# Kernel optimization log

Hardware: AMD Instinct MI355X
Metric: run time of the kernel (lower is better)

## Reference

```python
import jax, jax.numpy as jnp
import numpy as np

C = 512
HEADS = 8
B, H, W = 2, 64, 64


def setup_inputs() -> dict:
    key = jax.random.key(0)
    k1, k2, k3, k4, k5 = jax.random.split(key, 5)
    s = 1.0 / np.sqrt(C)
    return {
        "hidden_states": jax.random.normal(k1, (B, C, H, W), dtype=jnp.float32),
        "qkv_w": jax.random.normal(k2, (3 * C, C), dtype=jnp.float32) * s,
        "qkv_b": jax.random.normal(k3, (3 * C,), dtype=jnp.float32) * 0.02,
        "proj_w": jax.random.normal(k4, (C, C), dtype=jnp.float32) * s,
        "proj_b": jax.random.normal(k5, (C,), dtype=jnp.float32) * 0.02,
    }


def reference(hidden_states, qkv_w, qkv_b, proj_w, proj_b):
    b, c, h, w = hidden_states.shape
    n = h * w  # sequence length
    heads = HEADS
    dim_head = c // heads
    scale = dim_head ** -0.5

    x = hidden_states.reshape(b, c, n)  # [b, c, n]
    # 1x1 conv1d == matmul over channel dim
    qkv = jnp.einsum("oc,bcn->bon", qkv_w, x) + qkv_b[None, :, None]  # [b, 3c, n]
    q, k, v = jnp.split(qkv, 3, axis=1)
    # [b, heads, dim_head, n] -> [b, heads, n, dim_head]
    def split_heads(t):
        return t.reshape(b, heads, dim_head, n).transpose(0, 1, 3, 2)
    q, k, v = split_heads(q), split_heads(k), split_heads(v)

    attn = jnp.einsum("bhqd,bhkd->bhqk", q, k) * scale  # [b, heads, n, n]
    attn = jax.nn.softmax(attn, axis=-1)
    out = jnp.einsum("bhqk,bhkd->bhqd", attn, v)  # [b, heads, n, dim_head]
    out = out.transpose(0, 1, 3, 2).reshape(b, c, n)  # [b, c, n]
    out = jnp.einsum("oc,bcn->bon", proj_w, out) + proj_b[None, :, None]
    return out  # [b, c, h*w] (matches torch module, no reshape back)
```

## Files before the change

kernel.cpp:

```cpp
#include <hip/hip_runtime.h>


typedef __attribute__((ext_vector_type(8))) short s16x8;
typedef __attribute__((ext_vector_type(4))) float f32x4;
typedef __attribute__((ext_vector_type(4))) unsigned short u16x4;

__device__ __forceinline__ unsigned short f2bf(float f) {
  unsigned u = __builtin_bit_cast(unsigned, f);
  u += 0x7fffu + ((u >> 16) & 1u);
  return (unsigned short)(u >> 16);
}

__device__ __forceinline__ unsigned cvt_pk_bf16(float lo, float hi) {
  unsigned r;
  asm("v_cvt_pk_bf16_f32 %0, %1, %2" : "=v"(r) : "v"(lo), "v"(hi));
  return r;
}

__global__ __launch_bounds__(256) void prep_weights(
    const float* __restrict__ qkv_w, const float* __restrict__ proj_w,
    short* __restrict__ wq, short* __restrict__ wp) {
  int t = blockIdx.x * 256 + threadIdx.x;
  const int NQ = 1536 * 512 / 4;
  if (t < NQ) {
    float4 v = ((const float4*)qkv_w)[t];
    u16x4 o; o[0] = f2bf(v.x); o[1] = f2bf(v.y); o[2] = f2bf(v.z); o[3] = f2bf(v.w);
    ((u16x4*)wq)[t] = o;
  } else {
    int t2 = t - NQ;
    float4 v = ((const float4*)proj_w)[t2];
    u16x4 o; o[0] = f2bf(v.x); o[1] = f2bf(v.y); o[2] = f2bf(v.z); o[3] = f2bf(v.w);
    ((u16x4*)wp)[t2] = o;
  }
}

__global__ __launch_bounds__(256) void prep_transpose(
    const float* __restrict__ x, short* __restrict__ xt) {
  __shared__ short TL[64 * 72];
  const int b = blockIdx.z, c0 = blockIdx.y * 64, n0 = blockIdx.x * 64;
  const int t = threadIdx.x;
  const int cr = t >> 4, n4 = (t & 15) * 4;
#pragma unroll
  for (int i = 0; i < 4; i++) {
    int c = cr + i * 16;
    float4 v = *(const float4*)(x + ((size_t)(b * 512 + c0 + c)) * 4096 + n0 + n4);
    TL[(n4 + 0) * 72 + c] = (short)f2bf(v.x);
    TL[(n4 + 1) * 72 + c] = (short)f2bf(v.y);
    TL[(n4 + 2) * 72 + c] = (short)f2bf(v.z);
    TL[(n4 + 3) * 72 + c] = (short)f2bf(v.w);
  }
  __syncthreads();
  const int n = t >> 2;
#pragma unroll
  for (int s2 = 0; s2 < 2; s2++) {
    int s = (t & 3) * 2 + s2;
    s16x8 v = *(const s16x8*)&TL[n * 72 + s * 8];
    *(s16x8*)(xt + ((size_t)(b * 4096 + n0 + n)) * 512 + c0 + s * 8) = v;
  }
}

__global__ __launch_bounds__(256) void qkv_gemm(
    const short* __restrict__ wq, const short* __restrict__ xt,
    const float* __restrict__ qkv_b,
    short* __restrict__ qkbuf,
    short* __restrict__ vbuf) {
  __shared__ short Al[128 * 40];
  __shared__ short Bl[128 * 40];
  const int b = blockIdx.z;
  const int m0 = blockIdx.y * 128, n0 = blockIdx.x * 128;
  const bool swapped = (blockIdx.y < 8);
  const int t = threadIdx.x, lane = t & 63, wid = t >> 6;
  const int wr = wid >> 1, wc = wid & 1;
  const int srow = t >> 1, scol = (t & 1) * 16;
  const short* gA = wq + (size_t)(m0 + srow) * 512 + scol;
  const short* gB = xt + ((size_t)(b * 4096 + n0 + srow)) * 512 + scol;
  short* lA = &Al[srow * 40 + scol];
  short* lB = &Bl[srow * 40 + scol];
  const short* As = swapped ? Bl : Al;
  const short* Bs = swapped ? Al : Bl;
  f32x4 acc[4][4] = {};
  for (int ks = 0; ks < 16; ks++) {
    *(s16x8*)lA       = *(const s16x8*)(gA + ks * 32);
    *(s16x8*)(lA + 8) = *(const s16x8*)(gA + ks * 32 + 8);
    *(s16x8*)lB       = *(const s16x8*)(gB + ks * 32);
    *(s16x8*)(lB + 8) = *(const s16x8*)(gB + ks * 32 + 8);
    __syncthreads();
    s16x8 af[4], bf[4];
#pragma unroll
    for (int i = 0; i < 4; i++) {
      af[i] = *(const s16x8*)&As[(wr * 64 + i * 16 + (lane & 15)) * 40 + ((lane >> 4) << 3)];
      bf[i] = *(const s16x8*)&Bs[(wc * 64 + i * 16 + (lane & 15)) * 40 + ((lane >> 4) << 3)];
    }
#pragma unroll
    for (int i = 0; i < 4; i++)
#pragma unroll
      for (int j = 0; j < 4; j++)
        acc[i][j] = __builtin_amdgcn_mfma_f32_16x16x32_bf16(af[i], bf[j], acc[i][j], 0, 0, 0);
    __syncthreads();
  }
  if (!swapped) {
#pragma unroll
    for (int i = 0; i < 4; i++)
#pragma unroll
      for (int r = 0; r < 4; r++) {
        int orow = m0 + wr * 64 + i * 16 + ((lane >> 4) << 2) + r;
        float bias = qkv_b[orow];
#pragma unroll
        for (int j = 0; j < 4; j++) {
          int ncol = n0 + wc * 64 + j * 16 + (lane & 15);
          vbuf[((size_t)(b * 512 + orow - 1024)) * 4096 + ncol] = (short)f2bf(acc[i][j][r] + bias);
        }
      }
  } else {
    const float qs = (m0 < 512) ? 0.18033688f : 1.0f;
#pragma unroll
    for (int j = 0; j < 4; j++) {
      int ocol = m0 + wc * 64 + j * 16 + (lane & 15);
      float bias = qkv_b[ocol];
#pragma unroll
      for (int i = 0; i < 4; i++)
#pragma unroll
        for (int r = 0; r < 4; r++) {
          int nrow = n0 + wr * 64 + i * 16 + ((lane >> 4) << 2) + r;
          qkbuf[((size_t)(b * 4096 + nrow)) * 1024 + ocol] = (short)f2bf((acc[i][j][r] + bias) * qs);
        }
    }
  }
}

__global__ __launch_bounds__(512) void flash_attn(
    const short* __restrict__ qkbuf, const short* __restrict__ vbuf,
    short* __restrict__ aout) {
  __shared__ short Kl[64 * 72];
  __shared__ short Vl[64 * 72];
  __shared__ short Pl[8 * 16 * 72];
  const int t = threadIdx.x, lane = t & 63, wid = t >> 6;
  const int g = lane >> 4, c = lane & 15;
  const int bh = blockIdx.y, b = bh >> 3, h = bh & 7;
  const int qrow = blockIdx.x * 128 + wid * 16 + c;

  s16x8 qf[2];
#pragma unroll
  for (int kd = 0; kd < 2; kd++)
    qf[kd] = *(const s16x8*)(qkbuf + ((size_t)(b * 4096 + qrow)) * 1024
                             + h * 64 + kd * 32 + g * 8);

  f32x4 oacc[4] = {};
  float m = -__builtin_inff();
  float l = 0.f;

  const int srow = t >> 3, sseg = (t & 7) * 8;
  const short* gK = qkbuf + ((size_t)(b * 4096 + srow)) * 1024 + 512 + h * 64 + sseg;
  const short* gV = vbuf + ((size_t)(b * 512 + h * 64 + srow)) * 4096 + sseg;
  short* lK = &Kl[srow * 72 + sseg];
  short* lV = &Vl[srow * 72 + sseg];
  short* myP = &Pl[wid * 16 * 72];

  s16x8 rK = *(const s16x8*)gK;
  s16x8 rV = *(const s16x8*)gV;

  for (int kt = 0; kt < 64; kt++) {
    *(s16x8*)lK = rK;
    *(s16x8*)lV = rV;
    __syncthreads();
    if (kt < 63) {
      rK = *(const s16x8*)(gK + (size_t)(kt + 1) * 64 * 1024);
      rV = *(const s16x8*)(gV + (kt + 1) * 64);
    }
    s16x8 kf[4][2];
#pragma unroll
    for (int ni = 0; ni < 4; ni++)
#pragma unroll
      for (int kd = 0; kd < 2; kd++)
        kf[ni][kd] = *(const s16x8*)&Kl[(ni * 16 + c) * 72 + kd * 32 + g * 8];
    f32x4 st[4] = {};
#pragma unroll
    for (int ni = 0; ni < 4; ni++) {
      st[ni] = __builtin_amdgcn_mfma_f32_16x16x32_bf16(kf[ni][0], qf[0], st[ni], 0, 0, 0);
      st[ni] = __builtin_amdgcn_mfma_f32_16x16x32_bf16(kf[ni][1], qf[1], st[ni], 0, 0, 0);
    }
    float t01 = fmaxf(fmaxf(st[0][0], st[0][1]), fmaxf(st[0][2], st[0][3]));
    float t23 = fmaxf(fmaxf(st[1][0], st[1][1]), fmaxf(st[1][2], st[1][3]));
    float t45 = fmaxf(fmaxf(st[2][0], st[2][1]), fmaxf(st[2][2], st[2][3]));
    float t67 = fmaxf(fmaxf(st[3][0], st[3][1]), fmaxf(st[3][2], st[3][3]));
    float tm = fmaxf(fmaxf(t01, t23), fmaxf(t45, t67));
    tm = fmaxf(tm, __shfl_xor(tm, 16));
    tm = fmaxf(tm, __shfl_xor(tm, 32));
    if (!__all(tm <= m + 8.f)) {
      float mn = fmaxf(m, tm);
      float alpha = exp2f(m - mn);
      m = mn;
      l *= alpha;
#pragma unroll
      for (int di = 0; di < 4; di++)
#pragma unroll
        for (int r = 0; r < 4; r++) oacc[di][r] *= alpha;
    }
    float ps = 0.f;
#pragma unroll
    for (int ni = 0; ni < 4; ni++) {
      float p0 = exp2f(st[ni][0] - m);
      float p1 = exp2f(st[ni][1] - m);
      float p2 = exp2f(st[ni][2] - m);
      float p3 = exp2f(st[ni][3] - m);
      ps += (p0 + p1) + (p2 + p3);
      uint2 w;
      w.x = cvt_pk_bf16(p0, p1);
      w.y = cvt_pk_bf16(p2, p3);
      *(uint2*)&myP[c * 72 + ni * 16 + g * 4] = w;
    }
    l += ps;
#pragma unroll
    for (int ks = 0; ks < 2; ks++) {
      s16x8 pa = *(const s16x8*)&myP[c * 72 + ks * 32 + g * 8];
      s16x8 vbf[4];
#pragma unroll
      for (int di = 0; di < 4; di++)
        vbf[di] = *(const s16x8*)&Vl[(di * 16 + c) * 72 + ks * 32 + g * 8];
#pragma unroll
      for (int di = 0; di < 4; di++)
        oacc[di] = __builtin_amdgcn_mfma_f32_16x16x32_bf16(vbf[di], pa, oacc[di], 0, 0, 0);
    }
    __syncthreads();
  }
  float lf = l;
  lf += __shfl_xor(lf, 16);
  lf += __shfl_xor(lf, 32);
  float inv = 1.f / lf;
#pragma unroll
  for (int di = 0; di < 4; di++)
#pragma unroll
    for (int r = 0; r < 4; r++) {
      int d = di * 16 + g * 4 + r;
      aout[((size_t)(b * 4096 + qrow)) * 512 + h * 64 + d] = (short)f2bf(oacc[di][r] * inv);
    }
}

__global__ __launch_bounds__(256) void proj_gemm(
    const short* __restrict__ wp, const short* __restrict__ aout,
    const float* __restrict__ proj_b, float* __restrict__ out) {
  __shared__ short Al[128 * 40];
  __shared__ short Bl[128 * 40];
  const int b = blockIdx.z;
  const int m0 = blockIdx.y * 128, n0 = blockIdx.x * 128;
  const int t = threadIdx.x, lane = t & 63, wid = t >> 6;
  const int wr = wid >> 1, wc = wid & 1;
  const int srow = t >> 1, scol = (t & 1) * 16;
  const short* gA = wp + (size_t)(m0 + srow) * 512 + scol;
  const short* gB = aout + ((size_t)(b * 4096 + n0 + srow)) * 512 + scol;
  short* lA = &Al[srow * 40 + scol];
  short* lB = &Bl[srow * 40 + scol];
  f32x4 acc[4][4] = {};
  for (int ks = 0; ks < 16; ks++) {
    *(s16x8*)lA       = *(const s16x8*)(gA + ks * 32);
    *(s16x8*)(lA + 8) = *(const s16x8*)(gA + ks * 32 + 8);
    *(s16x8*)lB       = *(const s16x8*)(gB + ks * 32);
    *(s16x8*)(lB + 8) = *(const s16x8*)(gB + ks * 32 + 8);
    __syncthreads();
    s16x8 af[4], bf[4];
#pragma unroll
    for (int i = 0; i < 4; i++) {
      af[i] = *(const s16x8*)&Al[(wr * 64 + i * 16 + (lane & 15)) * 40 + ((lane >> 4) << 3)];
      bf[i] = *(const s16x8*)&Bl[(wc * 64 + i * 16 + (lane & 15)) * 40 + ((lane >> 4) << 3)];
    }
#pragma unroll
    for (int i = 0; i < 4; i++)
#pragma unroll
      for (int j = 0; j < 4; j++)
        acc[i][j] = __builtin_amdgcn_mfma_f32_16x16x32_bf16(af[i], bf[j], acc[i][j], 0, 0, 0);
    __syncthreads();
  }
#pragma unroll
  for (int i = 0; i < 4; i++)
#pragma unroll
    for (int r = 0; r < 4; r++) {
      int orow = m0 + wr * 64 + i * 16 + ((lane >> 4) << 2) + r;
      float bias = proj_b[orow];
#pragma unroll
      for (int j = 0; j < 4; j++) {
        int ncol = n0 + wc * 64 + j * 16 + (lane & 15);
        out[((size_t)(b * 512 + orow)) * 4096 + ncol] = acc[i][j][r] + bias;
      }
    }
}

extern "C" void kernel_launch(void* const* d_in, const int* in_sizes, int n_in,
                              void* d_out, int out_size, void* d_ws, size_t ws_size,
                              hipStream_t stream) {
  const float* x      = (const float*)d_in[0];
  const float* qkv_w  = (const float*)d_in[1];
  const float* qkv_b  = (const float*)d_in[2];
  const float* proj_w = (const float*)d_in[3];
  const float* proj_b = (const float*)d_in[4];
  float* out = (float*)d_out;
  char* ws = (char*)d_ws;
  short* wq = (short*)(ws);
  short* wp = (short*)(ws + 1572864);
  short* xt = (short*)(ws + 2097152);
  short* qk = (short*)(ws + 10485760);
  short* vb = (short*)(ws + 27262976);
  short* ao = (short*)(ws + 35651584);

  prep_weights  <<<1024, 256, 0, stream>>>(qkv_w, proj_w, wq, wp);
  prep_transpose<<<dim3(64, 8, 2), 256, 0, stream>>>(x, xt);
  qkv_gemm      <<<dim3(32, 12, 2), 256, 0, stream>>>(wq, xt, qkv_b, qk, vb);
  flash_attn    <<<dim3(32, 16), 512, 0, stream>>>(qk, vb, ao);
  proj_gemm     <<<dim3(32, 4, 2), 256, 0, stream>>>(wp, ao, proj_b, out);
}
```

Before: 253.8 us.

## Restructure flash attention: direct K/V register loads, 32 query rows per wave, no LDS staging

The flash attention kernel now uses 256-thread blocks in which each wave handles 32 query rows (two 16-row MFMA tiles). K and V tiles are loaded straight from global memory into registers instead of being staged through shared memory behind __syncthreads, which removes the block-wide barriers. Each K/V fragment is reused across both query tiles. The per-wave P buffer uses an XOR swizzle in place of padding, blocks are remapped so heads are interleaved across workgroups, and output stores are packed into 8-byte writes. The cost is that each wave issues its own global loads for K/V (relying on L2 for sharing) and register pressure rises.

```diff
diff --git a/kernel.cpp b/kernel.cpp
--- a/kernel.cpp
+++ b/kernel.cpp
@@ -128,112 +128,117 @@
   }
 }
 
-__global__ __launch_bounds__(512) void flash_attn(
+__global__ __launch_bounds__(256) void flash_attn(
     const short* __restrict__ qkbuf, const short* __restrict__ vbuf,
     short* __restrict__ aout) {
-  __shared__ short Kl[64 * 72];
-  __shared__ short Vl[64 * 72];
-  __shared__ short Pl[8 * 16 * 72];
+  __shared__ short Pl[4 * 32 * 64];
   const int t = threadIdx.x, lane = t & 63, wid = t >> 6;
   const int g = lane >> 4, c = lane & 15;
-  const int bh = blockIdx.y, b = bh >> 3, h = bh & 7;
-  const int qrow = blockIdx.x * 128 + wid * 16 + c;
-
-  s16x8 qf[2];
-#pragma unroll
-  for (int kd = 0; kd < 2; kd++)
-    qf[kd] = *(const s16x8*)(qkbuf + ((size_t)(b * 4096 + qrow)) * 1024
-                             + h * 64 + kd * 32 + g * 8);
-
-  f32x4 oacc[4] = {};
-  float m = -__builtin_inff();
-  float l = 0.f;
-
-  const int srow = t >> 3, sseg = (t & 7) * 8;
-  const short* gK = qkbuf + ((size_t)(b * 4096 + srow)) * 1024 + 512 + h * 64 + sseg;
-  const short* gV = vbuf + ((size_t)(b * 512 + h * 64 + srow)) * 4096 + sseg;
-  short* lK = &Kl[srow * 72 + sseg];
-  short* lV = &Vl[srow * 72 + sseg];
-  short* myP = &Pl[wid * 16 * 72];
-
-  s16x8 rK = *(const s16x8*)gK;
-  s16x8 rV = *(const s16x8*)gV;
+  const int j = blockIdx.x;
+  const int lid = ((j & 7) << 6) + (j >> 3);
+  const int qb = (lid & 31) * 128 + wid * 32;
+  const int bh = lid >> 5, b = bh >> 3, h = bh & 7;
+
+  s16x8 qf[2][2];
+#pragma unroll
+  for (int mi = 0; mi < 2; mi++)
+#pragma unroll
+    for (int kd = 0; kd < 2; kd++)
+      qf[mi][kd] = *(const s16x8*)(qkbuf + ((size_t)(b * 4096 + qb + mi * 16 + c)) * 1024
+                                   + h * 64 + kd * 32 + g * 8);
+
+  f32x4 oacc[2][4] = {};
+  float m[2] = {-__builtin_inff(), -__builtin_inff()};
+  float l[2] = {0.f, 0.f};
+
+  const short* kbase = qkbuf + ((size_t)(b * 4096 + c)) * 1024 + 512 + h * 64 + g * 8;
+  const short* vbase = vbuf + ((size_t)(b * 512 + h * 64 + c)) * 4096 + g * 8;
+  short* myP = &Pl[wid * 32 * 64];
+  const int sw = (c & 7) << 3;
 
   for (int kt = 0; kt < 64; kt++) {
-    *(s16x8*)lK = rK;
-    *(s16x8*)lV = rV;
-    __syncthreads();
-    if (kt < 63) {
-      rK = *(const s16x8*)(gK + (size_t)(kt + 1) * 64 * 1024);
-      rV = *(const s16x8*)(gV + (kt + 1) * 64);
-    }
-    s16x8 kf[4][2];
+    const int kp0 = kt * 64;
+    s16x8 kf[4][2], vf[2][4];
 #pragma unroll
     for (int ni = 0; ni < 4; ni++)
 #pragma unroll
       for (int kd = 0; kd < 2; kd++)
-        kf[ni][kd] = *(const s16x8*)&Kl[(ni * 16 + c) * 72 + kd * 32 + g * 8];
-    f32x4 st[4] = {};
-#pragma unroll
-    for (int ni = 0; ni < 4; ni++) {
-      st[ni] = __builtin_amdgcn_mfma_f32_16x16x32_bf16(kf[ni][0], qf[0], st[ni], 0, 0, 0);
-      st[ni] = __builtin_amdgcn_mfma_f32_16x16x32_bf16(kf[ni][1], qf[1], st[ni], 0, 0, 0);
-    }
-    float t01 = fmaxf(fmaxf(st[0][0], st[0][1]), fmaxf(st[0][2], st[0][3]));
-    float t23 = fmaxf(fmaxf(st[1][0], st[1][1]), fmaxf(st[1][2], st[1][3]));
-    float t45 = fmaxf(fmaxf(st[2][0], st[2][1]), fmaxf(st[2][2], st[2][3]));
-    float t67 = fmaxf(fmaxf(st[3][0], st[3][1]), fmaxf(st[3][2], st[3][3]));
-    float tm = fmaxf(fmaxf(t01, t23), fmaxf(t45, t67));
-    tm = fmaxf(tm, __shfl_xor(tm, 16));
-    tm = fmaxf(tm, __shfl_xor(tm, 32));
-    if (!__all(tm <= m + 8.f)) {
-      float mn = fmaxf(m, tm);
-      float alpha = exp2f(m - mn);
-      m = mn;
-      l *= alpha;
+        kf[ni][kd] = *(const s16x8*)(kbase + (size_t)(kp0 + ni * 16) * 1024 + kd * 32);
+#pragma unroll
+    for (int ks = 0; ks < 2; ks++)
 #pragma unroll
       for (int di = 0; di < 4; di++)
-#pragma unroll
-        for (int r = 0; r < 4; r++) oacc[di][r] *= alpha;
-    }
-    float ps = 0.f;
-#pragma unroll
-    for (int ni = 0; ni < 4; ni++) {
-      float p0 = exp2f(st[ni][0] - m);
-      float p1 = exp2f(st[ni][1] - m);
-      float p2 = exp2f(st[ni][2] - m);
-      float p3 = exp2f(st[ni][3] - m);
-      ps += (p0 + p1) + (p2 + p3);
+        vf[ks][di] = *(const s16x8*)(vbase + (size_t)(di * 16) * 4096 + kp0 + ks * 32);
+#pragma unroll
+    for (int mi = 0; mi < 2; mi++) {
+      f32x4 st[4] = {};
+#pragma unroll
+      for (int ni = 0; ni < 4; ni++) {
+        st[ni] = __builtin_amdgcn_mfma_f32_16x16x32_bf16(kf[ni][0], qf[mi][0], st[ni], 0, 0, 0);
+        st[ni] = __builtin_amdgcn_mfma_f32_16x16x32_bf16(kf[ni][1], qf[mi][1], st[ni], 0, 0, 0);
+      }
+      float t01 = fmaxf(fmaxf(st[0][0], st[0][1]), fmaxf(st[0][2], st[0][3]));
+      float t23 = fmaxf(fmaxf(st[1][0], st[1][1]), fmaxf(st[1][2], st[1][3]));
+      float t45 = fmaxf(fmaxf(st[2][0], st[2][1]), fmaxf(st[2][2], st[2][3]));
+      float t67 = fmaxf(fmaxf(st[3][0], st[3][1]), fmaxf(st[3][2], st[3][3]));
+      float tm = fmaxf(fmaxf(t01, t23), fmaxf(t45, t67));
+      tm = fmaxf(tm, __shfl_xor(tm, 16));
+      tm = fmaxf(tm, __shfl_xor(tm, 32));
+      if (!__all(tm <= m[mi] + 8.f)) {
+        float mn = fmaxf(m[mi], tm);
+        float alpha = exp2f(m[mi] - mn);
+        m[mi] = mn;
+        l[mi] *= alpha;
+#pragma unroll
+        for (int di = 0; di < 4; di++)
+#pragma unroll
+          for (int r = 0; r < 4; r++) oacc[mi][di][r] *= alpha;
+      }
+      float ps = 0.f;
+      const int prow = (mi * 16 + c) * 64;
+#pragma unroll
+      for (int ni = 0; ni < 4; ni++) {
+        float p0 = exp2f(st[ni][0] - m[mi]);
+        float p1 = exp2f(st[ni][1] - m[mi]);
+        float p2 = exp2f(st[ni][2] - m[mi]);
+        float p3 = exp2f(st[ni][3] - m[mi]);
+        ps += (p0 + p1) + (p2 + p3);
+        uint2 w;
+        w.x = cvt_pk_bf16(p0, p1);
+        w.y = cvt_pk_bf16(p2, p3);
+        *(uint2*)&myP[prow + ((ni * 16 + g * 4) ^ sw)] = w;
+      }
+      l[mi] += ps;
+    }
+#pragma unroll
+    for (int ks = 0; ks < 2; ks++) {
+      s16x8 pa[2];
+#pragma unroll
+      for (int mi = 0; mi < 2; mi++)
+        pa[mi] = *(const s16x8*)&myP[(mi * 16 + c) * 64 + ((ks * 32 + g * 8) ^ sw)];
+#pragma unroll
+      for (int di = 0; di < 4; di++) {
+#pragma unroll
+        for (int mi = 0; mi < 2; mi++)
+          oacc[mi][di] = __builtin_amdgcn_mfma_f32_16x16x32_bf16(vf[ks][di], pa[mi], oacc[mi][di], 0, 0, 0);
+      }
+    }
+  }
+#pragma unroll
+  for (int mi = 0; mi < 2; mi++) {
+    float lf = l[mi];
+    lf += __shfl_xor(lf, 16);
+    lf += __shfl_xor(lf, 32);
+    float inv = 1.f / lf;
+    const size_t orow = ((size_t)(b * 4096 + qb + mi * 16 + c)) * 512 + h * 64;
+#pragma unroll
+    for (int di = 0; di < 4; di++) {
       uint2 w;
-      w.x = cvt_pk_bf16(p0, p1);
-      w.y = cvt_pk_bf16(p2, p3);
-      *(uint2*)&myP[c * 72 + ni * 16 + g * 4] = w;
-    }
-    l += ps;
-#pragma unroll
-    for (int ks = 0; ks < 2; ks++) {
-      s16x8 pa = *(const s16x8*)&myP[c * 72 + ks * 32 + g * 8];
-      s16x8 vbf[4];
-#pragma unroll
-      for (int di = 0; di < 4; di++)
-        vbf[di] = *(const s16x8*)&Vl[(di * 16 + c) * 72 + ks * 32 + g * 8];
-#pragma unroll
-      for (int di = 0; di < 4; di++)
-        oacc[di] = __builtin_amdgcn_mfma_f32_16x16x32_bf16(vbf[di], pa, oacc[di], 0, 0, 0);
-    }
-    __syncthreads();
-  }
-  float lf = l;
-  lf += __shfl_xor(lf, 16);
-  lf += __shfl_xor(lf, 32);
-  float inv = 1.f / lf;
-#pragma unroll
-  for (int di = 0; di < 4; di++)
-#pragma unroll
-    for (int r = 0; r < 4; r++) {
-      int d = di * 16 + g * 4 + r;
-      aout[((size_t)(b * 4096 + qrow)) * 512 + h * 64 + d] = (short)f2bf(oacc[di][r] * inv);
-    }
+      w.x = cvt_pk_bf16(oacc[mi][di][0] * inv, oacc[mi][di][1] * inv);
+      w.y = cvt_pk_bf16(oacc[mi][di][2] * inv, oacc[mi][di][3] * inv);
+      *(uint2*)(aout + orow + di * 16 + g * 4) = w;
+    }
+  }
 }
 
 __global__ __launch_bounds__(256) void proj_gemm(
@@ -304,6 +309,6 @@
   prep_weights  <<<1024, 256, 0, stream>>>(qkv_w, proj_w, wq, wp);
   prep_transpose<<<dim3(64, 8, 2), 256, 0, stream>>>(x, xt);
   qkv_gemm      <<<dim3(32, 12, 2), 256, 0, stream>>>(wq, xt, qkv_b, qk, vb);
-  flash_attn    <<<dim3(32, 16), 512, 0, stream>>>(qk, vb, ao);
+  flash_attn    <<<512, 256, 0, stream>>>(qk, vb, ao);
   proj_gemm     <<<dim3(32, 4, 2), 256, 0, stream>>>(wp, ao, proj_b, out);
 }
```

Result: slower. 354.2 us (+39.5%).

## Rewrite flash attention with 32x32 MFMA, register P exchange, and swizzled LDS

Applied to the files above, without the earlier changes.

The attention kernel moves from 16x16x32 to 32x32x16 bf16 MFMA tiles, with each wave handling 32 query rows in a 256-thread block. The P matrix is now passed between lanes with permlane32_swap instead of a round trip through shared memory. K and V tiles use an XOR-swizzled 64-wide LDS layout in place of padding, and block IDs are remapped so consecutive blocks spread across heads. The goal is to cut LDS traffic and instruction count per tile, at the cost of more register pressure from the larger accumulators.

```diff
diff --git a/kernel.cpp b/kernel.cpp
--- a/kernel.cpp
+++ b/kernel.cpp
@@ -3,7 +3,10 @@
 
 typedef __attribute__((ext_vector_type(8))) short s16x8;
 typedef __attribute__((ext_vector_type(4))) float f32x4;
+typedef __attribute__((ext_vector_type(16))) float f32x16;
 typedef __attribute__((ext_vector_type(4))) unsigned short u16x4;
+typedef __attribute__((ext_vector_type(2))) unsigned u32x2;
+typedef __attribute__((ext_vector_type(4))) unsigned u32x4;
 
 __device__ __forceinline__ unsigned short f2bf(float f) {
   unsigned u = __builtin_bit_cast(unsigned, f);
@@ -128,111 +131,112 @@
   }
 }
 
-__global__ __launch_bounds__(512) void flash_attn(
+__global__ __launch_bounds__(256) void flash_attn(
     const short* __restrict__ qkbuf, const short* __restrict__ vbuf,
     short* __restrict__ aout) {
-  __shared__ short Kl[64 * 72];
-  __shared__ short Vl[64 * 72];
-  __shared__ short Pl[8 * 16 * 72];
+  __shared__ short Kl[64 * 64];
+  __shared__ short Vl[64 * 64];
   const int t = threadIdx.x, lane = t & 63, wid = t >> 6;
-  const int g = lane >> 4, c = lane & 15;
-  const int bh = blockIdx.y, b = bh >> 3, h = bh & 7;
-  const int qrow = blockIdx.x * 128 + wid * 16 + c;
-
-  s16x8 qf[2];
-#pragma unroll
-  for (int kd = 0; kd < 2; kd++)
-    qf[kd] = *(const s16x8*)(qkbuf + ((size_t)(b * 4096 + qrow)) * 1024
-                             + h * 64 + kd * 32 + g * 8);
-
-  f32x4 oacc[4] = {};
+  const int hi = lane >> 5, q32 = lane & 31;
+  const int j = blockIdx.x;
+  const int lid = ((j & 7) << 6) + (j >> 3);
+  const int qb = (lid & 31) * 128 + wid * 32;
+  const int bh = lid >> 5, b = bh >> 3, h = bh & 7;
+
+  s16x8 qf[4];
+  {
+    const short* qrow = qkbuf + ((size_t)(b * 4096 + qb + q32)) * 1024 + h * 64 + hi * 8;
+#pragma unroll
+    for (int dc = 0; dc < 4; dc++) qf[dc] = *(const s16x8*)(qrow + dc * 16);
+  }
+
+  f32x16 oacc[2] = {};
   float m = -__builtin_inff();
   float l = 0.f;
 
-  const int srow = t >> 3, sseg = (t & 7) * 8;
-  const short* gK = qkbuf + ((size_t)(b * 4096 + srow)) * 1024 + 512 + h * 64 + sseg;
-  const short* gV = vbuf + ((size_t)(b * 512 + h * 64 + srow)) * 4096 + sseg;
-  short* lK = &Kl[srow * 72 + sseg];
-  short* lV = &Vl[srow * 72 + sseg];
-  short* myP = &Pl[wid * 16 * 72];
-
-  s16x8 rK = *(const s16x8*)gK;
-  s16x8 rV = *(const s16x8*)gV;
+  const int srow = t >> 2;
+  const int swz = (srow & 7) << 4;
+  const int o0 = ((t & 3) * 32) ^ swz;
+  const int o1 = ((t & 3) * 32 + 16) ^ swz;
+  const short* gK = qkbuf + ((size_t)(b * 4096 + srow)) * 1024 + 512 + h * 64 + (t & 3) * 16;
+  const short* gV = vbuf + ((size_t)(b * 512 + h * 64 + srow)) * 4096 + (t & 3) * 16;
+  char* lKrow = (char*)&Kl[srow * 64];
+  char* lVrow = (char*)&Vl[srow * 64];
+
+  s16x8 pk0 = *(const s16x8*)gK, pk1 = *(const s16x8*)(gK + 8);
+  s16x8 pv0 = *(const s16x8*)gV, pv1 = *(const s16x8*)(gV + 8);
 
   for (int kt = 0; kt < 64; kt++) {
-    *(s16x8*)lK = rK;
-    *(s16x8*)lV = rV;
+    *(s16x8*)(lKrow + o0) = pk0;  *(s16x8*)(lKrow + o1) = pk1;
+    *(s16x8*)(lVrow + o0) = pv0;  *(s16x8*)(lVrow + o1) = pv1;
     __syncthreads();
     if (kt < 63) {
-      rK = *(const s16x8*)(gK + (size_t)(kt + 1) * 64 * 1024);
-      rV = *(const s16x8*)(gV + (kt + 1) * 64);
-    }
-    s16x8 kf[4][2];
-#pragma unroll
-    for (int ni = 0; ni < 4; ni++)
-#pragma unroll
-      for (int kd = 0; kd < 2; kd++)
-        kf[ni][kd] = *(const s16x8*)&Kl[(ni * 16 + c) * 72 + kd * 32 + g * 8];
-    f32x4 st[4] = {};
-#pragma unroll
-    for (int ni = 0; ni < 4; ni++) {
-      st[ni] = __builtin_amdgcn_mfma_f32_16x16x32_bf16(kf[ni][0], qf[0], st[ni], 0, 0, 0);
-      st[ni] = __builtin_amdgcn_mfma_f32_16x16x32_bf16(kf[ni][1], qf[1], st[ni], 0, 0, 0);
-    }
-    float t01 = fmaxf(fmaxf(st[0][0], st[0][1]), fmaxf(st[0][2], st[0][3]));
-    float t23 = fmaxf(fmaxf(st[1][0], st[1][1]), fmaxf(st[1][2], st[1][3]));
-    float t45 = fmaxf(fmaxf(st[2][0], st[2][1]), fmaxf(st[2][2], st[2][3]));
-    float t67 = fmaxf(fmaxf(st[3][0], st[3][1]), fmaxf(st[3][2], st[3][3]));
-    float tm = fmaxf(fmaxf(t01, t23), fmaxf(t45, t67));
-    tm = fmaxf(tm, __shfl_xor(tm, 16));
-    tm = fmaxf(tm, __shfl_xor(tm, 32));
-    if (!__all(tm <= m + 8.f)) {
-      float mn = fmaxf(m, tm);
-      float alpha = exp2f(m - mn);
-      m = mn;
-      l *= alpha;
-#pragma unroll
-      for (int di = 0; di < 4; di++)
-#pragma unroll
-        for (int r = 0; r < 4; r++) oacc[di][r] *= alpha;
-    }
-    float ps = 0.f;
-#pragma unroll
-    for (int ni = 0; ni < 4; ni++) {
-      float p0 = exp2f(st[ni][0] - m);
-      float p1 = exp2f(st[ni][1] - m);
-      float p2 = exp2f(st[ni][2] - m);
-      float p3 = exp2f(st[ni][3] - m);
-      ps += (p0 + p1) + (p2 + p3);
+      const short* nK = gK + (size_t)(kt + 1) * 64 * 1024;
+      const short* nV = gV + (kt + 1) * 64;
+      pk0 = *(const s16x8*)nK;  pk1 = *(const s16x8*)(nK + 8);
+      pv0 = *(const s16x8*)nV;  pv1 = *(const s16x8*)(nV + 8);
+    }
+#pragma unroll
+    for (int kb = 0; kb < 2; kb++) {
+      f32x16 st = {};
+      const int krow = kb * 32 + q32;
+      const int ksw = (krow & 7) << 4;
+#pragma unroll
+      for (int dc = 0; dc < 4; dc++) {
+        s16x8 kf = *(const s16x8*)((char*)&Kl[krow * 64] + ((dc * 32 + hi * 16) ^ ksw));
+        st = __builtin_amdgcn_mfma_f32_32x32x16_bf16(kf, qf[dc], st, 0, 0, 0);
+      }
+      float tm = st[0];
+#pragma unroll
+      for (int r2 = 1; r2 < 16; r2++) tm = fmaxf(tm, st[r2]);
+      tm = fmaxf(tm, __shfl_xor(tm, 32));
+      if (!__all(tm <= m + 8.f)) {
+        float mn = fmaxf(m, tm);
+        float alpha = exp2f(m - mn);
+        m = mn;
+        l *= alpha;
+#pragma unroll
+        for (int di = 0; di < 2; di++)
+#pragma unroll
+          for (int r2 = 0; r2 < 16; r2++) oacc[di][r2] *= alpha;
+      }
+      float p[16];
+      float ps = 0.f;
+#pragma unroll
+      for (int r2 = 0; r2 < 16; r2++) { p[r2] = exp2f(st[r2] - m); ps += p[r2]; }
+      l += ps;
+#pragma unroll
+      for (int kh = 0; kh < 2; kh++) {
+        unsigned A  = cvt_pk_bf16(p[kh * 8 + 0], p[kh * 8 + 1]);
+        unsigned Bu = cvt_pk_bf16(p[kh * 8 + 4], p[kh * 8 + 5]);
+        unsigned C  = cvt_pk_bf16(p[kh * 8 + 2], p[kh * 8 + 3]);
+        unsigned D  = cvt_pk_bf16(p[kh * 8 + 6], p[kh * 8 + 7]);
+        u32x2 r0 = __builtin_amdgcn_permlane32_swap(A, Bu, false, false);
+        u32x2 r1 = __builtin_amdgcn_permlane32_swap(C, D, false, false);
+        u32x4 uu; uu[0] = r0[0]; uu[1] = r1[0]; uu[2] = r0[1]; uu[3] = r1[1];
+        s16x8 pf = __builtin_bit_cast(s16x8, uu);
+#pragma unroll
+        for (int di = 0; di < 2; di++) {
+          const int vrow = di * 32 + q32;
+          s16x8 vf = *(const s16x8*)((char*)&Vl[vrow * 64]
+                       + ((kb * 64 + kh * 32 + hi * 16) ^ ((vrow & 7) << 4)));
+          oacc[di] = __builtin_amdgcn_mfma_f32_32x32x16_bf16(vf, pf, oacc[di], 0, 0, 0);
+        }
+      }
+    }
+    __syncthreads();
+  }
+  l += __shfl_xor(l, 32);
+  float inv = 1.f / l;
+  short* orow = aout + ((size_t)(b * 4096 + qb + q32)) * 512 + h * 64;
+#pragma unroll
+  for (int di = 0; di < 2; di++)
+#pragma unroll
+    for (int blk = 0; blk < 4; blk++) {
       uint2 w;
-      w.x = cvt_pk_bf16(p0, p1);
-      w.y = cvt_pk_bf16(p2, p3);
-      *(uint2*)&myP[c * 72 + ni * 16 + g * 4] = w;
-    }
-    l += ps;
-#pragma unroll
-    for (int ks = 0; ks < 2; ks++) {
-      s16x8 pa = *(const s16x8*)&myP[c * 72 + ks * 32 + g * 8];
-      s16x8 vbf[4];
-#pragma unroll
-      for (int di = 0; di < 4; di++)
-        vbf[di] = *(const s16x8*)&Vl[(di * 16 + c) * 72 + ks * 32 + g * 8];
-#pragma unroll
-      for (int di = 0; di < 4; di++)
-        oacc[di] = __builtin_amdgcn_mfma_f32_16x16x32_bf16(vbf[di], pa, oacc[di], 0, 0, 0);
-    }
-    __syncthreads();
-  }
-  float lf = l;
-  lf += __shfl_xor(lf, 16);
-  lf += __shfl_xor(lf, 32);
-  float inv = 1.f / lf;
-#pragma unroll
-  for (int di = 0; di < 4; di++)
-#pragma unroll
-    for (int r = 0; r < 4; r++) {
-      int d = di * 16 + g * 4 + r;
-      aout[((size_t)(b * 4096 + qrow)) * 512 + h * 64 + d] = (short)f2bf(oacc[di][r] * inv);
+      w.x = cvt_pk_bf16(oacc[di][blk * 4 + 0] * inv, oacc[di][blk * 4 + 1] * inv);
+      w.y = cvt_pk_bf16(oacc[di][blk * 4 + 2] * inv, oacc[di][blk * 4 + 3] * inv);
+      *(uint2*)(orow + di * 32 + blk * 8 + hi * 4) = w;
     }
 }
 
@@ -304,6 +308,6 @@
   prep_weights  <<<1024, 256, 0, stream>>>(qkv_w, proj_w, wq, wp);
   prep_transpose<<<dim3(64, 8, 2), 256, 0, stream>>>(x, xt);
   qkv_gemm      <<<dim3(32, 12, 2), 256, 0, stream>>>(wq, xt, qkv_b, qk, vb);
-  flash_attn    <<<dim3(32, 16), 512, 0, stream>>>(qk, vb, ao);
+  flash_attn    <<<512, 256, 0, stream>>>(qk, vb, ao);
   proj_gemm     <<<dim3(32, 4, 2), 256, 0, stream>>>(wp, ao, proj_b, out);
 }
```

Measured after the change: 265.7 us. 1.05x slower.
